# Kernel tuning notes

Measured on AMD Instinct MI355X. Metric: run time of the kernel, lower is better.

## Reference

```python
import jax, jax.numpy as jnp
import numpy as np

GRID_LO = 32
GRID_HI = 128
NF = 4          # n_features
K = 9           # num_neighbors
NUM_CLASSES = 36
BS = 128
P_LO = GRID_LO * GRID_LO   # 1024
P_HI = GRID_HI * GRID_HI   # 16384


def _knn_neighbor_indices():
    """Replicates cKDTree(lo_coords).query(hi_coords, k=K)[1]: lo grid has
    spacing ratio=grid_hi//grid_lo, hi grid spacing 1; neighbors sorted by
    distance (stable sort -> ties broken by lower linear index)."""
    ratio = GRID_HI // GRID_LO
    lo = np.stack(np.meshgrid(np.arange(GRID_LO) * ratio,
                              np.arange(GRID_LO) * ratio, indexing='ij'),
                  axis=-1).reshape(-1, 2).astype(np.float64)   # (P_LO, 2)
    hi = np.stack(np.meshgrid(np.arange(GRID_HI),
                              np.arange(GRID_HI), indexing='ij'),
                  axis=-1).reshape(-1, 2).astype(np.float64)   # (P_HI, 2)
    d2 = ((hi[:, None, :] - lo[None, :, :]) ** 2).sum(-1)      # (P_HI, P_LO)
    idx = np.argsort(d2, axis=1, kind='stable')[:, :K]          # (P_HI, K)
    return jnp.asarray(idx, dtype=jnp.int32)


def setup_inputs() -> dict:
    key = jax.random.key(0)
    k1, k2, k3, k4, k5 = jax.random.split(key, 5)
    x = jax.random.normal(k1, (BS, NF * P_LO), dtype=jnp.float32)
    cls_ids = jax.random.randint(k2, (BS,), 0, NUM_CLASSES)
    neighbor_indices = _knn_neighbor_indices()                  # (P_HI, K)
    weight_map = jax.random.normal(k3, (NUM_CLASSES, NF, P_HI, K), dtype=jnp.float32) * 0.05
    bias_low = jax.random.normal(k4, (NUM_CLASSES, NF, P_LO), dtype=jnp.float32) * 0.05
    bias_high = jax.random.normal(k5, (NUM_CLASSES, NF, P_HI), dtype=jnp.float32) * 0.05
    return {"x": x, "cls_ids": cls_ids, "neighbor_indices": neighbor_indices,
            "weight_map": weight_map, "bias_low": bias_low, "bias_high": bias_high}


def reference(x, cls_ids, neighbor_indices, weight_map, bias_low, bias_high):
    # x: (BS, NF*P_LO) -> (BS, NF, P_LO)
    y_low = x.reshape(x.shape[0], NF, P_LO)
    y_low_db = y_low - bias_low[cls_ids]                        # (BS, NF, P_LO)
    # gather k=9 lo-res neighbors for every hi-res pixel (all features at once)
    neigh = y_low_db[:, :, neighbor_indices]                    # (BS, NF, P_HI, K)
    weights = weight_map[cls_ids]                               # (BS, NF, P_HI, K)
    out = jnp.einsum('bfpk,bfpk->bfp', neigh, weights)          # weighted sum over k
    out = out + bias_high[cls_ids]                              # (BS, NF, P_HI)
    return out.reshape(x.shape[0], NF, GRID_HI, GRID_HI)
```

## Files before the change

### kernel.cpp

```cpp
#include <hip/hip_runtime.h>

#define BS      128
#define NF      4
#define NC      36
#define P_LO    1024
#define P_HI    16384
#define KNN     9
#define THREADS 256
#define TILE_P  512
#define TILE_F  (TILE_P * KNN)
#define NTILES  (P_HI / TILE_P)
#define LIST_OFF 64

__global__ __launch_bounds__(128) void build_lists_kernel(
    const int* __restrict__ cls_ids, int* __restrict__ ws)
{
    __shared__ int cnt[NC];
    const int t = threadIdx.x;
    if (t < NC) cnt[t] = 0;
    __syncthreads();
    if (t < BS) {
        int c = cls_ids[t];
        int pos = atomicAdd(&cnt[c], 1);
        ws[LIST_OFF + c * BS + pos] = t;
    }
    __syncthreads();
    if (t < NC) ws[t] = cnt[t];
}

__global__ __launch_bounds__(THREADS) void rect_up_kernel(
    const float* __restrict__ x,
    const int*   __restrict__ ws,
    const int*   __restrict__ nbr,
    const float* __restrict__ wmap,
    const float* __restrict__ blo,
    const float* __restrict__ bhi,
    float*       __restrict__ out)
{
    __shared__ __align__(16) char smem[TILE_F * 4 * 2];
    float* w_st = (float*)smem;
    int*   i_st = (int*)(smem + TILE_F * 4);
    float* ybuf = (float*)(smem + TILE_F * 4);

    const int tile = blockIdx.x % NTILES;
    const int cf   = blockIdx.x / NTILES;
    const int f    = cf % NF;
    const int cls  = cf / NF;

    const int n_b = ws[cls];
    if (n_b == 0) return;

    const int tid   = threadIdx.x;
    const int tbase = tile * TILE_P;

    const float4* wsrc = (const float4*)(wmap + ((size_t)(cls * NF + f) * P_HI + tbase) * KNN);
    const int4*   isrc = (const int4*)(nbr + (size_t)tbase * KNN);
    float4* w4 = (float4*)w_st;
    int4*   i4 = (int4*)i_st;
    #pragma unroll
    for (int i = tid; i < TILE_F / 4; i += THREADS) {
        w4[i] = wsrc[i];
        i4[i] = isrc[i];
    }
    __syncthreads();

    float w[18]; int nb[18];
    {
        const float2* wr = (const float2*)w_st + (size_t)tid * 9;
        const int2*   ir = (const int2*)i_st + (size_t)tid * 9;
        #pragma unroll
        for (int j = 0; j < 9; ++j) {
            float2 a = wr[j]; w[2 * j] = a.x; w[2 * j + 1] = a.y;
            int2   c = ir[j]; nb[2 * j] = c.x; nb[2 * j + 1] = c.y;
        }
    }
    __syncthreads();

    const int    p0 = tbase + 2 * tid;
    const float2 bh = *(const float2*)(bhi + (size_t)(cls * NF + f) * P_HI + p0);
    const float4 bl = ((const float4*)(blo + (cls * NF + f) * P_LO))[tid];
    const int*  list = ws + LIST_OFF + cls * BS;

    {
        const int b = list[0];
        float4 xv = ((const float4*)(x + (b * NF + f) * P_LO))[tid];
        float4 r;
        r.x = xv.x - bl.x; r.y = xv.y - bl.y;
        r.z = xv.z - bl.z; r.w = xv.w - bl.w;
        ((float4*)ybuf)[tid] = r;
    }

    for (int s = 0; s < n_b; ++s) {
        __syncthreads();
        const float* y = ybuf + (s & 1) * P_LO;
        if (s + 1 < n_b) {
            const int b1 = list[s + 1];
            float4 xv = ((const float4*)(x + (b1 * NF + f) * P_LO))[tid];
            float4 r;
            r.x = xv.x - bl.x; r.y = xv.y - bl.y;
            r.z = xv.z - bl.z; r.w = xv.w - bl.w;
            ((float4*)(ybuf + ((s + 1) & 1) * P_LO))[tid] = r;
        }
        const int b = list[s];
        float a0 = 0.f, a1 = 0.f;
        #pragma unroll
        for (int k = 0; k < 9; ++k) a0 = fmaf(w[k],     y[nb[k]],     a0);
        #pragma unroll
        for (int k = 0; k < 9; ++k) a1 = fmaf(w[9 + k], y[nb[9 + k]], a1);
        float2 o;
        o.x = a0 + bh.x;
        o.y = a1 + bh.y;
        *(float2*)(out + (size_t)(b * NF + f) * P_HI + p0) = o;
    }
}

extern "C" void kernel_launch(void* const* d_in, const int* in_sizes, int n_in,
                              void* d_out, int out_size, void* d_ws, size_t ws_size,
                              hipStream_t stream) {
    const float* x    = (const float*)d_in[0];
    const int*   cls  = (const int*)d_in[1];
    const int*   nbr  = (const int*)d_in[2];
    const float* wmap = (const float*)d_in[3];
    const float* blo  = (const float*)d_in[4];
    const float* bhi  = (const float*)d_in[5];
    float*       out  = (float*)d_out;
    int*         wsl  = (int*)d_ws;

    build_lists_kernel<<<1, 128, 0, stream>>>(cls, wsl);
    rect_up_kernel<<<NC * NF * NTILES, THREADS, 0, stream>>>(
        x, wsl, nbr, wmap, blo, bhi, out);
}
```

Before: 167.0 us.

## Stage only needed low-res rows and batch samples in groups of eight

Each tile now loads only the 192-element window of low-res pixels its neighbors can touch (rebased indices) instead of all 1024, and shares one staging buffer between indices and weights to shrink shared memory. Samples are processed in groups of 8 with one sync per group instead of double buffering with a sync per sample. This cuts global reads of x and the bias, raises occupancy through lower LDS use, and reduces barrier count, at the cost of extra sync phases during setup and a fixed window assumption tied to the grid geometry.

```diff
diff --git a/kernel.cpp b/kernel.cpp
--- a/kernel.cpp
+++ b/kernel.cpp
@@ -10,6 +10,8 @@
 #define TILE_P  512
 #define TILE_F  (TILE_P * KNN)
 #define NTILES  (P_HI / TILE_P)
+#define SGRP    8
+#define YROWS   192
 #define LIST_OFF 64
 
 __global__ __launch_bounds__(128) void build_lists_kernel(
@@ -37,10 +39,9 @@
     const float* __restrict__ bhi,
     float*       __restrict__ out)
 {
-    __shared__ __align__(16) char smem[TILE_F * 4 * 2];
-    float* w_st = (float*)smem;
-    int*   i_st = (int*)(smem + TILE_F * 4);
-    float* ybuf = (float*)(smem + TILE_F * 4);
+    __shared__ __align__(16) int   stage[TILE_F];
+    __shared__ __align__(16) float bl_s[YROWS];
+    __shared__ __align__(16) float ybuf[SGRP * YROWS];
 
     const int tile = blockIdx.x % NTILES;
     const int cf   = blockIdx.x / NTILES;
@@ -50,67 +51,88 @@
     const int n_b = ws[cls];
     if (n_b == 0) return;
 
-    const int tid   = threadIdx.x;
-    const int tbase = tile * TILE_P;
+    const int tid = threadIdx.x;
+    int start = tile - 2;
+    if (start < 0)  start = 0;
+    if (start > 26) start = 26;
+    const int rebase = start * 32;
 
-    const float4* wsrc = (const float4*)(wmap + ((size_t)(cls * NF + f) * P_HI + tbase) * KNN);
-    const int4*   isrc = (const int4*)(nbr + (size_t)tbase * KNN);
-    float4* w4 = (float4*)w_st;
-    int4*   i4 = (int4*)i_st;
-    #pragma unroll
-    for (int i = tid; i < TILE_F / 4; i += THREADS) {
-        w4[i] = wsrc[i];
-        i4[i] = isrc[i];
-    }
+    const int4* isrc = (const int4*)(nbr + (size_t)tile * TILE_P * KNN);
+    for (int i = tid; i < TILE_F / 4; i += THREADS)
+        ((int4*)stage)[i] = isrc[i];
     __syncthreads();
 
-    float w[18]; int nb[18];
+    int nb[18];
     {
-        const float2* wr = (const float2*)w_st + (size_t)tid * 9;
-        const int2*   ir = (const int2*)i_st + (size_t)tid * 9;
+        const int2* ir = (const int2*)stage + (size_t)tid * 9;
         #pragma unroll
         for (int j = 0; j < 9; ++j) {
-            float2 a = wr[j]; w[2 * j] = a.x; w[2 * j + 1] = a.y;
-            int2   c = ir[j]; nb[2 * j] = c.x; nb[2 * j + 1] = c.y;
+            int2 c = ir[j];
+            nb[2 * j]     = c.x - rebase;
+            nb[2 * j + 1] = c.y - rebase;
         }
     }
     __syncthreads();
 
-    const int    p0 = tbase + 2 * tid;
-    const float2 bh = *(const float2*)(bhi + (size_t)(cls * NF + f) * P_HI + p0);
-    const float4 bl = ((const float4*)(blo + (cls * NF + f) * P_LO))[tid];
-    const int*  list = ws + LIST_OFF + cls * BS;
+    const float4* wsrc = (const float4*)(wmap +
+        ((size_t)(cls * NF + f) * P_HI + (size_t)tile * TILE_P) * KNN);
+    float* w_st = (float*)stage;
+    for (int i = tid; i < TILE_F / 4; i += THREADS)
+        ((float4*)w_st)[i] = wsrc[i];
+    if (tid < YROWS / 4)
+        ((float4*)bl_s)[tid] =
+            ((const float4*)(blo + (cls * NF + f) * P_LO + rebase))[tid];
+    __syncthreads();
 
+    float wl[18];
     {
-        const int b = list[0];
-        float4 xv = ((const float4*)(x + (b * NF + f) * P_LO))[tid];
-        float4 r;
-        r.x = xv.x - bl.x; r.y = xv.y - bl.y;
-        r.z = xv.z - bl.z; r.w = xv.w - bl.w;
-        ((float4*)ybuf)[tid] = r;
+        const float2* wr = (const float2*)w_st + (size_t)tid * 9;
+        #pragma unroll
+        for (int j = 0; j < 9; ++j) {
+            float2 a = wr[j];
+            wl[2 * j]     = a.x;
+            wl[2 * j + 1] = a.y;
+        }
     }
 
-    for (int s = 0; s < n_b; ++s) {
+    const int    p0   = tile * TILE_P + 2 * tid;
+    const float2 bh   = *(const float2*)(bhi + (size_t)(cls * NF + f) * P_HI + p0);
+    const int*   list = ws + LIST_OFF + cls * BS;
+
+    for (int g = 0; g < n_b; g += SGRP) {
+        const int cnt = min(SGRP, n_b - g);
         __syncthreads();
-        const float* y = ybuf + (s & 1) * P_LO;
-        if (s + 1 < n_b) {
-            const int b1 = list[s + 1];
-            float4 xv = ((const float4*)(x + (b1 * NF + f) * P_LO))[tid];
-            float4 r;
-            r.x = xv.x - bl.x; r.y = xv.y - bl.y;
-            r.z = xv.z - bl.z; r.w = xv.w - bl.w;
-            ((float4*)(ybuf + ((s + 1) & 1) * P_LO))[tid] = r;
+        {
+            const int si = tid >> 5;
+            const int el = tid & 31;
+            if (si < cnt) {
+                const int    b  = list[g + si];
+                const float4* xs = (const float4*)(x + (b * NF + f) * P_LO + rebase);
+                #pragma unroll
+                for (int i = el; i < YROWS / 4; i += 32) {
+                    float4 xv = xs[i];
+                    float4 bv = ((const float4*)bl_s)[i];
+                    float4 r;
+                    r.x = xv.x - bv.x; r.y = xv.y - bv.y;
+                    r.z = xv.z - bv.z; r.w = xv.w - bv.w;
+                    ((float4*)ybuf)[si * (YROWS / 4) + i] = r;
+                }
+            }
         }
-        const int b = list[s];
-        float a0 = 0.f, a1 = 0.f;
-        #pragma unroll
-        for (int k = 0; k < 9; ++k) a0 = fmaf(w[k],     y[nb[k]],     a0);
-        #pragma unroll
-        for (int k = 0; k < 9; ++k) a1 = fmaf(w[9 + k], y[nb[9 + k]], a1);
-        float2 o;
-        o.x = a0 + bh.x;
-        o.y = a1 + bh.y;
-        *(float2*)(out + (size_t)(b * NF + f) * P_HI + p0) = o;
+        __syncthreads();
+        for (int s = 0; s < cnt; ++s) {
+            const float* y = ybuf + s * YROWS;
+            const int    b = list[g + s];
+            float a0 = 0.f, a1 = 0.f;
+            #pragma unroll
+            for (int j = 0; j < 9; ++j) a0 = fmaf(wl[j],     y[nb[j]],     a0);
+            #pragma unroll
+            for (int j = 0; j < 9; ++j) a1 = fmaf(wl[9 + j], y[nb[9 + j]], a1);
+            float2 o;
+            o.x = a0 + bh.x;
+            o.y = a1 + bh.y;
+            *(float2*)(out + (size_t)(b * NF + f) * P_HI + p0) = o;
+        }
     }
 }
 
```

Result: slower. 171.4 us (+2.6%).
